# Performance work log

Measured on AMD Instinct MI355X. Metric: run time of the kernel, lower is better.

Reference implementation:

```python
import jax, jax.numpy as jnp
import numpy as np

EMBED_DIM = 1024
NUM_HEADS = 16
HEAD_DIM = EMBED_DIM // NUM_HEADS
NEG = -1000000000.0


def setup_inputs() -> dict:
    key = jax.random.key(0)
    ks = jax.random.split(key, 13)
    B, S, D = 4, 2048, EMBED_DIM
    scale = 1.0 / np.sqrt(D)
    inp = {
        "query": jax.random.normal(ks[0], (B, S, D), jnp.float32),
        "key": jax.random.normal(ks[1], (B, S, D), jnp.float32),
        "value": jax.random.normal(ks[2], (B, S, D), jnp.float32),
        "mask": jax.random.randint(ks[3], (B, 1, 1, S), 0, 2, jnp.int32),
        "Wq": jax.random.normal(ks[4], (D, D), jnp.float32) * scale,
        "bq": jnp.zeros((D,), jnp.float32),
        "Wk": jax.random.normal(ks[5], (D, D), jnp.float32) * scale,
        "bk": jnp.zeros((D,), jnp.float32),
        "Wv": jax.random.normal(ks[6], (D, D), jnp.float32) * scale,
        "bv": jnp.zeros((D,), jnp.float32),
        "Wo": jax.random.normal(ks[7], (D, D), jnp.float32) * scale,
        "bo": jnp.zeros((D,), jnp.float32),
    }
    return inp


def _split_heads(x):
    B, S, D = x.shape
    return x.reshape(B, S, NUM_HEADS, HEAD_DIM).transpose(0, 2, 1, 3)  # [B,H,S,hd]


def reference(query, key, value, mask, Wq, bq, Wk, bk, Wv, bv, Wo, bo):
    B, S, D = query.shape
    Q = _split_heads(query @ Wq + bq)
    K = _split_heads(key @ Wk + bk)
    V = _split_heads(value @ Wv + bv)
    scores = jnp.einsum("bhqd,bhkd->bhqk", Q, K) / jnp.sqrt(jnp.float32(HEAD_DIM))
    scores = jnp.where(mask == 0, jnp.float32(NEG), scores)
    attn = jax.nn.softmax(scores, axis=-1)
    out = jnp.einsum("bhqk,bhkd->bhqd", attn, V)
    out = out.transpose(0, 2, 1, 3).reshape(B, S, D)
    return out @ Wo + bo
```

## Files before the change

kernel.cpp:

```cpp
#include <hip/hip_runtime.h>


#define SEQ   2048
#define EDIM  1024
#define NHEAD 16
#define HDIM  64
#define NBAT  4
#define MTOK  8192

typedef __attribute__((ext_vector_type(8))) __bf16 bf16x8;
typedef __attribute__((ext_vector_type(4))) float f32x4;
typedef __attribute__((ext_vector_type(8))) unsigned short us8;
typedef unsigned short u16;

#define SCL   0.1803368801111244f
#define MADD_OK   (-12.0f)
#define MADD_MASK (-100000.0f)

__device__ __forceinline__ u16 bfbits(float f) {
    __bf16 h = (__bf16)f;
    return __builtin_bit_cast(u16, h);
}
__device__ __forceinline__ bf16x8 bc(us8 v) { return __builtin_bit_cast(bf16x8, v); }
__device__ __forceinline__ float exp2fast(float x) {
    float r;
    asm("v_exp_f32 %0, %1" : "=v"(r) : "v"(x));
    return r;
}

__global__ __launch_bounds__(256) void prep_kernel(const int* __restrict__ mask,
                                                   int* __restrict__ idxl,
                                                   int* __restrict__ cntp) {
    __shared__ int psum[257];
    const int b = blockIdx.x, t = threadIdx.x;
    const int* mp = mask + b * SEQ;
    int m8[8]; int s = 0;
#pragma unroll
    for (int i = 0; i < 8; ++i) { m8[i] = mp[t * 8 + i]; s += (m8[i] != 0); }
    psum[t + 1] = s;
    __syncthreads();
    if (t == 0) { psum[0] = 0; for (int i = 1; i <= 256; ++i) psum[i] += psum[i - 1]; }
    __syncthreads();
    int ex = psum[t];
#pragma unroll
    for (int i = 0; i < 8; ++i)
        if (m8[i] != 0) idxl[b * SEQ + (ex++)] = t * 8 + i;
    if (t == 0) cntp[b] = psum[256];
}

__global__ __launch_bounds__(256) void wtrans4_kernel(const float* __restrict__ W0,
                                                      const float* __restrict__ W1,
                                                      const float* __restrict__ W2,
                                                      const float* __restrict__ W3,
                                                      u16* __restrict__ WT) {
    __shared__ float tile[32][33];
    const int tx = threadIdx.x, ty = threadIdx.y;
    const int bx = blockIdx.x,  by = blockIdx.y, wz = blockIdx.z;
    const float* W = (wz == 0) ? W0 : (wz == 1) ? W1 : (wz == 2) ? W2 : W3;
    u16* O = WT + (size_t)wz * EDIM * EDIM;
#pragma unroll
    for (int i = 0; i < 4; ++i)
        tile[ty + i * 8][tx] = W[(size_t)(by * 32 + ty + i * 8) * EDIM + bx * 32 + tx];
    __syncthreads();
#pragma unroll
    for (int i = 0; i < 4; ++i) {
        int n = bx * 32 + ty + i * 8;
        int k = by * 32 + tx;
        O[(size_t)n * EDIM + k] = bfbits(tile[tx][ty + i * 8]);
    }
}

template <int MODE, bool ABF16, bool GATHER>
__global__ __launch_bounds__(256) void gemm_kernel(const void* __restrict__ Ap,
                                                   const u16* __restrict__ WT,
                                                   const float* __restrict__ bias,
                                                   void* __restrict__ outp,
                                                   const int* __restrict__ idxl,
                                                   const int* __restrict__ cntp) {
    const int bm = blockIdx.x, bn = blockIdx.y;
    int cn = 0;
    if constexpr (GATHER) {
        cn = cntp[bm >> 4];
        if (((bm & 15) * 128) >= cn) return;
    }

    __shared__ u16 As[128][56];
    __shared__ u16 Bs[128][56];

    const int tid  = threadIdx.x;
    const int lane = tid & 63, wave = tid >> 6;
    const int g    = lane >> 4, l15 = lane & 15;
    const int wrow = wave >> 1, wcol = wave & 1;
    const int tr   = tid >> 1, tk = (tid & 1) * 16;

    int arow;
    if constexpr (GATHER) {
        const int sloc = (bm & 15) * 128 + tr;
        const int gi = (sloc < cn) ? idxl[(bm >> 4) * SEQ + sloc] : 0;
        arow = (bm >> 4) * SEQ + gi;
    } else {
        arow = bm * 128 + tr;
    }

    f32x4 acc[4][4] = {};

    bf16x8 sa0, sa1, sb0, sb1;
    auto LOAD = [&](int k0) {
        if constexpr (ABF16) {
            const u16* A = (const u16*)Ap;
            const u16* p = A + (size_t)arow * EDIM + k0 + tk;
            sa0 = bc(*(const us8*)p);
            sa1 = bc(*(const us8*)(p + 8));
        } else {
            const float* A = (const float*)Ap;
            const float* p = A + (size_t)arow * EDIM + k0 + tk;
            f32x4 v0 = *(const f32x4*)p;
            f32x4 v1 = *(const f32x4*)(p + 4);
            f32x4 v2 = *(const f32x4*)(p + 8);
            f32x4 v3 = *(const f32x4*)(p + 12);
#pragma unroll
            for (int j = 0; j < 4; ++j) {
                sa0[j] = (__bf16)v0[j]; sa0[4 + j] = (__bf16)v1[j];
                sa1[j] = (__bf16)v2[j]; sa1[4 + j] = (__bf16)v3[j];
            }
        }
        const u16* q = WT + (size_t)(bn * 128 + tr) * EDIM + k0 + tk;
        sb0 = bc(*(const us8*)q);
        sb1 = bc(*(const us8*)(q + 8));
    };

    LOAD(0);
#pragma unroll 1
    for (int kt = 0; kt < EDIM / 32; ++kt) {
        __syncthreads();
        *(bf16x8*)&As[tr][tk]     = sa0;
        *(bf16x8*)&As[tr][tk + 8] = sa1;
        *(bf16x8*)&Bs[tr][tk]     = sb0;
        *(bf16x8*)&Bs[tr][tk + 8] = sb1;
        __syncthreads();
        if (kt < EDIM / 32 - 1) LOAD((kt + 1) * 32);

        bf16x8 af[4], bfr[4];
#pragma unroll
        for (int i = 0; i < 4; ++i)
            af[i] = bc(*(const us8*)&As[wrow * 64 + i * 16 + l15][g * 8]);
#pragma unroll
        for (int j = 0; j < 4; ++j)
            bfr[j] = bc(*(const us8*)&Bs[wcol * 64 + j * 16 + l15][g * 8]);
#pragma unroll
        for (int i = 0; i < 4; ++i)
#pragma unroll
            for (int j = 0; j < 4; ++j)
                acc[i][j] = __builtin_amdgcn_mfma_f32_16x16x32_bf16(af[i], bfr[j], acc[i][j], 0, 0, 0);
    }

#pragma unroll
    for (int i = 0; i < 4; ++i) {
#pragma unroll
        for (int j = 0; j < 4; ++j) {
            const int gm0 = bm * 128 + wrow * 64 + i * 16 + g * 4;
            const int gn  = bn * 128 + wcol * 64 + j * 16 + l15;
            const float bv = bias[gn];
#pragma unroll
            for (int r = 0; r < 4; ++r) {
                float val = acc[i][j][r] + bv;
                const int m = gm0 + r;
                if constexpr (GATHER) {
                    if ((m & 2047) >= cn) val = 0.f;
                }
                if constexpr (MODE == 2) {
                    ((float*)outp)[(size_t)m * EDIM + gn] = val;
                } else {
                    const int b = m >> 11, s = m & 2047;
                    const int h = gn >> 6, d = gn & 63;
                    u16* O = (u16*)outp;
                    if constexpr (MODE == 0)
                        O[((size_t)(b * NHEAD + h) << 17) + s * HDIM + d] = bfbits(val);
                    else
                        O[((size_t)(b * NHEAD + h) << 17) + d * SEQ + s] = bfbits(val);
                }
            }
        }
    }
}

__global__ __launch_bounds__(256) void attn_kernel(const u16* __restrict__ Q,
                                                   const u16* __restrict__ K,
                                                   const u16* __restrict__ VT,
                                                   const int* __restrict__ cntp,
                                                   u16* __restrict__ O) {
    __shared__ u16 Klds[2][64][72];
    __shared__ u16 Vlds[2][64][72];
    __shared__ float madd[SEQ];

    const int tid = threadIdx.x, lane = tid & 63, w = tid >> 6;
    const int g = lane >> 4, l15 = lane & 15;
    const int qb = blockIdx.x, bh = blockIdx.y;
    const int b = bh >> 4, h = bh & 15;

    const u16* Qp = Q + ((size_t)bh << 17);
    const u16* Kp = K + ((size_t)bh << 17);
    const u16* Vp = VT + ((size_t)bh << 17);
    const int q0 = qb * 64 + w * 16;

    const int cn  = cntp[b];
    const int ktc = (cn + 63) >> 6;

    for (int i = tid; i < ktc * 64; i += 256)
        madd[i] = (i < cn) ? MADD_OK : MADD_MASK;

    bf16x8 qf0 = bc(*(const us8*)&Qp[(size_t)(q0 + l15) * HDIM + g * 8]);
    bf16x8 qf1 = bc(*(const us8*)&Qp[(size_t)(q0 + l15) * HDIM + 32 + g * 8]);

    f32x4 ot[4] = {};
    float lsum = 0.f;

    const int sr = tid >> 2, scol = (tid & 3) * 16;
    const int kRow = ((l15 >> 2) << 3) + (l15 & 3);
    const f32x4 zf = {0.f, 0.f, 0.f, 0.f};

    {
        us8 a = *(const us8*)&Kp[(size_t)sr * HDIM + scol];
        us8 bq_ = *(const us8*)&Kp[(size_t)sr * HDIM + scol + 8];
        us8 c = *(const us8*)&Vp[(size_t)sr * SEQ + scol];
        us8 d = *(const us8*)&Vp[(size_t)sr * SEQ + scol + 8];
        *(us8*)&Klds[0][sr][scol]     = a;
        *(us8*)&Klds[0][sr][scol + 8] = bq_;
        *(us8*)&Vlds[0][sr][scol]     = c;
        *(us8*)&Vlds[0][sr][scol + 8] = d;
    }
    __syncthreads();

    for (int kt = 0; kt < ktc; ++kt) {
        const int cur = kt & 1;
        const int kbase = kt * 64;
        const bool more = (kt + 1) < ktc;

        us8 nk0, nk1, nv0, nv1;
        if (more) {
            const int nb = kbase + 64;
            nk0 = *(const us8*)&Kp[(size_t)(nb + sr) * HDIM + scol];
            nk1 = *(const us8*)&Kp[(size_t)(nb + sr) * HDIM + scol + 8];
            nv0 = *(const us8*)&Vp[(size_t)sr * SEQ + nb + scol];
            nv1 = *(const us8*)&Vp[(size_t)sr * SEQ + nb + scol + 8];
        }

        f32x4 st[4];
        const u16* Kb = &Klds[cur][0][0];
        __builtin_amdgcn_s_setprio(1);
#pragma unroll
        for (int u = 0; u < 4; ++u) {
            const int R = kRow + (u & 1) * 4 + (u >> 1) * 32;
            bf16x8 kf0 = bc(*(const us8*)&Kb[R * 72 + g * 8]);
            bf16x8 kf1 = bc(*(const us8*)&Kb[R * 72 + 32 + g * 8]);
            st[u] = __builtin_amdgcn_mfma_f32_16x16x32_bf16(kf0, qf0, zf, 0, 0, 0);
            st[u] = __builtin_amdgcn_mfma_f32_16x16x32_bf16(kf1, qf1, st[u], 0, 0, 0);
        }
        __builtin_amdgcn_s_setprio(0);

        float p[4][4];
#pragma unroll
        for (int u = 0; u < 4; ++u) {
            const f32x4 ma = *(const f32x4*)&madd[kbase + (u >> 1) * 32 + (u & 1) * 4 + g * 8];
#pragma unroll
            for (int r = 0; r < 4; ++r) {
                p[u][r] = exp2fast(fmaf(st[u][r], SCL, ma[r]));
                lsum += p[u][r];
            }
        }
        bf16x8 pf0, pf1;
#pragma unroll
        for (int j = 0; j < 4; ++j) {
            pf0[j]     = (__bf16)p[0][j];
            pf0[4 + j] = (__bf16)p[1][j];
            pf1[j]     = (__bf16)p[2][j];
            pf1[4 + j] = (__bf16)p[3][j];
        }

        const u16* Vb = &Vlds[cur][0][0];
        __builtin_amdgcn_s_setprio(1);
#pragma unroll
        for (int dblk = 0; dblk < 4; ++dblk) {
            bf16x8 vf0 = bc(*(const us8*)&Vb[(dblk * 16 + l15) * 72 + g * 8]);
            bf16x8 vf1 = bc(*(const us8*)&Vb[(dblk * 16 + l15) * 72 + 32 + g * 8]);
            ot[dblk] = __builtin_amdgcn_mfma_f32_16x16x32_bf16(vf0, pf0, ot[dblk], 0, 0, 0);
            ot[dblk] = __builtin_amdgcn_mfma_f32_16x16x32_bf16(vf1, pf1, ot[dblk], 0, 0, 0);
        }
        __builtin_amdgcn_s_setprio(0);

        if (more) {
            *(us8*)&Klds[cur ^ 1][sr][scol]     = nk0;
            *(us8*)&Klds[cur ^ 1][sr][scol + 8] = nk1;
            *(us8*)&Vlds[cur ^ 1][sr][scol]     = nv0;
            *(us8*)&Vlds[cur ^ 1][sr][scol + 8] = nv1;
        }
        __syncthreads();
    }

    lsum += __shfl_xor(lsum, 16);
    lsum += __shfl_xor(lsum, 32);
    const float inv = 1.f / lsum;

    const size_t row = (size_t)(b * SEQ + q0 + l15) * EDIM + h * HDIM;
#pragma unroll
    for (int dblk = 0; dblk < 4; ++dblk) {
#pragma unroll
        for (int j = 0; j < 2; ++j) {
            __attribute__((ext_vector_type(2))) __bf16 pr;
            pr[0] = (__bf16)(ot[dblk][2 * j] * inv);
            pr[1] = (__bf16)(ot[dblk][2 * j + 1] * inv);
            *(unsigned*)&O[row + dblk * 16 + g * 4 + 2 * j] = __builtin_bit_cast(unsigned, pr);
        }
    }
}

extern "C" void kernel_launch(void* const* d_in, const int* in_sizes, int n_in,
                              void* d_out, int out_size, void* d_ws, size_t ws_size,
                              hipStream_t stream) {
    const float* query = (const float*)d_in[0];
    const float* key   = (const float*)d_in[1];
    const float* value = (const float*)d_in[2];
    const int*   mask  = (const int*)d_in[3];
    const float* Wq = (const float*)d_in[4];  const float* bq = (const float*)d_in[5];
    const float* Wk = (const float*)d_in[6];  const float* bk = (const float*)d_in[7];
    const float* Wv = (const float*)d_in[8];  const float* bv = (const float*)d_in[9];
    const float* Wo = (const float*)d_in[10]; const float* bo = (const float*)d_in[11];

    char* ws = (char*)d_ws;
    const size_t WT_BYTES  = (size_t)EDIM * EDIM * 2;
    const size_t BUF_BYTES = (size_t)MTOK * EDIM * 2;
    u16* wtq   = (u16*)(ws);
    u16* wtk   = (u16*)(ws + WT_BYTES);
    u16* wtv   = (u16*)(ws + 2 * WT_BYTES);
    u16* wto   = (u16*)(ws + 3 * WT_BYTES);
    u16* Qbuf  = (u16*)(ws + 4 * WT_BYTES);
    u16* Kbuf  = (u16*)(ws + 4 * WT_BYTES + BUF_BYTES);
    u16* VTbuf = (u16*)(ws + 4 * WT_BYTES + 2 * BUF_BYTES);
    u16* Abuf  = (u16*)(ws + 4 * WT_BYTES + 3 * BUF_BYTES);
    int* idxl  = (int*)(ws + 4 * WT_BYTES + 4 * BUF_BYTES);
    int* cntp  = (int*)(ws + 4 * WT_BYTES + 4 * BUF_BYTES + (size_t)MTOK * 4);

    prep_kernel<<<NBAT, 256, 0, stream>>>(mask, idxl, cntp);

    dim3 tgrid(32, 32, 4), tblk(32, 8);
    wtrans4_kernel<<<tgrid, tblk, 0, stream>>>(Wq, Wk, Wv, Wo, wtq);

    dim3 ggrid(MTOK / 128, EDIM / 128);
    gemm_kernel<0, false, false><<<ggrid, 256, 0, stream>>>(query, wtq, bq, Qbuf, nullptr, nullptr);
    gemm_kernel<0, false, true ><<<ggrid, 256, 0, stream>>>(key,   wtk, bk, Kbuf, idxl, cntp);
    gemm_kernel<1, false, true ><<<ggrid, 256, 0, stream>>>(value, wtv, bv, VTbuf, idxl, cntp);

    dim3 agrid(SEQ / 64, NBAT * NHEAD);
    attn_kernel<<<agrid, 256, 0, stream>>>(Qbuf, Kbuf, VTbuf, cntp, Abuf);

    gemm_kernel<2, true, false><<<ggrid, 256, 0, stream>>>(Abuf, wto, bo, (float*)d_out, nullptr, nullptr);
}
```

Baseline: 215.7 us.

## Use 32x32x16 MFMA with XOR-swizzled LDS and remapped block order in attention

Rewrites the attention kernel to use 32x32x16 bf16 MFMA instructions, with each wave owning 32 query rows instead of 16. The block therefore covers 128 queries. The padded LDS tiles are replaced by unpadded 64x64 tiles with XOR swizzles to avoid bank conflicts. Blocks are launched as a 1D grid with a remap so that neighbouring blocks in launch order come from different batch-head pairs. The aim is to halve the K/V LDS traffic per query and reduce MFMA instruction count, at the cost of more accumulator registers and half as many blocks.

```diff
diff --git a/kernel.cpp b/kernel.cpp
--- a/kernel.cpp
+++ b/kernel.cpp
@@ -9,7 +9,9 @@
 #define MTOK  8192
 
 typedef __attribute__((ext_vector_type(8))) __bf16 bf16x8;
+typedef __attribute__((ext_vector_type(4))) __bf16 bf16x4;
 typedef __attribute__((ext_vector_type(4))) float f32x4;
+typedef __attribute__((ext_vector_type(16))) float f32x16;
 typedef __attribute__((ext_vector_type(8))) unsigned short us8;
 typedef unsigned short u16;
 
@@ -189,19 +191,22 @@
                                                    const u16* __restrict__ VT,
                                                    const int* __restrict__ cntp,
                                                    u16* __restrict__ O) {
-    __shared__ u16 Klds[2][64][72];
-    __shared__ u16 Vlds[2][64][72];
+    __shared__ u16 Klds[2][64][64];
+    __shared__ u16 Vlds[2][64][64];
     __shared__ float madd[SEQ];
 
     const int tid = threadIdx.x, lane = tid & 63, w = tid >> 6;
-    const int g = lane >> 4, l15 = lane & 15;
-    const int qb = blockIdx.x, bh = blockIdx.y;
-    const int b = bh >> 4, h = bh & 15;
+    const int h = lane >> 5, l31 = lane & 31;
+
+    const int id  = blockIdx.x;
+    const int bh  = (id & 7) * 8 + ((id >> 3) >> 4);
+    const int qb  = (id >> 3) & 15;
+    const int b   = bh >> 4, hd_ = bh & 15;
 
     const u16* Qp = Q + ((size_t)bh << 17);
     const u16* Kp = K + ((size_t)bh << 17);
     const u16* Vp = VT + ((size_t)bh << 17);
-    const int q0 = qb * 64 + w * 16;
+    const int q0w = qb * 128 + w * 32;
 
     const int cn  = cntp[b];
     const int ktc = (cn + 63) >> 6;
@@ -209,25 +214,34 @@
     for (int i = tid; i < ktc * 64; i += 256)
         madd[i] = (i < cn) ? MADD_OK : MADD_MASK;
 
-    bf16x8 qf0 = bc(*(const us8*)&Qp[(size_t)(q0 + l15) * HDIM + g * 8]);
-    bf16x8 qf1 = bc(*(const us8*)&Qp[(size_t)(q0 + l15) * HDIM + 32 + g * 8]);
-
-    f32x4 ot[4] = {};
+    bf16x8 qf[4];
+#pragma unroll
+    for (int khd = 0; khd < 4; ++khd)
+        qf[khd] = bc(*(const us8*)&Qp[(size_t)(q0w + l31) * HDIM + khd * 16 + h * 8]);
+
+    const int b_  = l31 & 3, hp = (l31 >> 2) & 1, cc = l31 >> 3;
+    const int piR = 16 * (cc & 1) + 8 * hp + 4 * (cc >> 1) + b_;
+    const int swk = (piR & 3) ^ (((piR >> 3) & 3) << 1);
+    const int swv = l31 & 7;
+
+    const int sr = tid >> 2, cu = (tid & 3) * 16;
+    const int ksw = ((sr & 3) ^ (((sr >> 3) & 3) << 1)) << 3;
+    const int vsw = (sr & 7) << 3;
+    const int kc0 = cu ^ ksw, kc1 = (cu + 8) ^ ksw;
+    const int vc0 = cu ^ vsw, vc1 = (cu + 8) ^ vsw;
+
+    f32x16 ot[2] = {};
     float lsum = 0.f;
 
-    const int sr = tid >> 2, scol = (tid & 3) * 16;
-    const int kRow = ((l15 >> 2) << 3) + (l15 & 3);
-    const f32x4 zf = {0.f, 0.f, 0.f, 0.f};
-
     {
-        us8 a = *(const us8*)&Kp[(size_t)sr * HDIM + scol];
-        us8 bq_ = *(const us8*)&Kp[(size_t)sr * HDIM + scol + 8];
-        us8 c = *(const us8*)&Vp[(size_t)sr * SEQ + scol];
-        us8 d = *(const us8*)&Vp[(size_t)sr * SEQ + scol + 8];
-        *(us8*)&Klds[0][sr][scol]     = a;
-        *(us8*)&Klds[0][sr][scol + 8] = bq_;
-        *(us8*)&Vlds[0][sr][scol]     = c;
-        *(us8*)&Vlds[0][sr][scol + 8] = d;
+        us8 a0 = *(const us8*)&Kp[(size_t)sr * HDIM + cu];
+        us8 a1 = *(const us8*)&Kp[(size_t)sr * HDIM + cu + 8];
+        us8 a2 = *(const us8*)&Vp[(size_t)sr * SEQ + cu];
+        us8 a3 = *(const us8*)&Vp[(size_t)sr * SEQ + cu + 8];
+        *(us8*)&Klds[0][sr][kc0] = a0;
+        *(us8*)&Klds[0][sr][kc1] = a1;
+        *(us8*)&Vlds[0][sr][vc0] = a2;
+        *(us8*)&Vlds[0][sr][vc1] = a3;
     }
     __syncthreads();
 
@@ -239,77 +253,85 @@
         us8 nk0, nk1, nv0, nv1;
         if (more) {
             const int nb = kbase + 64;
-            nk0 = *(const us8*)&Kp[(size_t)(nb + sr) * HDIM + scol];
-            nk1 = *(const us8*)&Kp[(size_t)(nb + sr) * HDIM + scol + 8];
-            nv0 = *(const us8*)&Vp[(size_t)sr * SEQ + nb + scol];
-            nv1 = *(const us8*)&Vp[(size_t)sr * SEQ + nb + scol + 8];
-        }
-
-        f32x4 st[4];
-        const u16* Kb = &Klds[cur][0][0];
+            nk0 = *(const us8*)&Kp[(size_t)(nb + sr) * HDIM + cu];
+            nk1 = *(const us8*)&Kp[(size_t)(nb + sr) * HDIM + cu + 8];
+            nv0 = *(const us8*)&Vp[(size_t)sr * SEQ + nb + cu];
+            nv1 = *(const us8*)&Vp[(size_t)sr * SEQ + nb + cu + 8];
+        }
+
+        f32x16 st[2] = {};
         __builtin_amdgcn_s_setprio(1);
 #pragma unroll
-        for (int u = 0; u < 4; ++u) {
-            const int R = kRow + (u & 1) * 4 + (u >> 1) * 32;
-            bf16x8 kf0 = bc(*(const us8*)&Kb[R * 72 + g * 8]);
-            bf16x8 kf1 = bc(*(const us8*)&Kb[R * 72 + 32 + g * 8]);
-            st[u] = __builtin_amdgcn_mfma_f32_16x16x32_bf16(kf0, qf0, zf, 0, 0, 0);
-            st[u] = __builtin_amdgcn_mfma_f32_16x16x32_bf16(kf1, qf1, st[u], 0, 0, 0);
+        for (int kb2 = 0; kb2 < 2; ++kb2) {
+            const u16* Kr = &Klds[cur][kb2 * 32 + piR][0];
+#pragma unroll
+            for (int khd = 0; khd < 4; ++khd) {
+                bf16x8 kf = bc(*(const us8*)&Kr[(khd * 16 + h * 8) ^ (swk << 3)]);
+                st[kb2] = __builtin_amdgcn_mfma_f32_32x32x16_bf16(kf, qf[khd], st[kb2], 0, 0, 0);
+            }
         }
         __builtin_amdgcn_s_setprio(0);
 
-        float p[4][4];
-#pragma unroll
-        for (int u = 0; u < 4; ++u) {
-            const f32x4 ma = *(const f32x4*)&madd[kbase + (u >> 1) * 32 + (u & 1) * 4 + g * 8];
-#pragma unroll
-            for (int r = 0; r < 4; ++r) {
-                p[u][r] = exp2fast(fmaf(st[u][r], SCL, ma[r]));
-                lsum += p[u][r];
-            }
-        }
-        bf16x8 pf0, pf1;
-#pragma unroll
-        for (int j = 0; j < 4; ++j) {
-            pf0[j]     = (__bf16)p[0][j];
-            pf0[4 + j] = (__bf16)p[1][j];
-            pf1[j]     = (__bf16)p[2][j];
-            pf1[4 + j] = (__bf16)p[3][j];
-        }
-
-        const u16* Vb = &Vlds[cur][0][0];
+        float pv[2][16];
+#pragma unroll
+        for (int kb2 = 0; kb2 < 2; ++kb2) {
+#pragma unroll
+            for (int cp = 0; cp < 4; ++cp) {
+                const f32x4 ma = *(const f32x4*)&madd[kbase + kb2 * 32 + 16 * (cp & 1) + 4 * (cp >> 1) + 8 * h];
+#pragma unroll
+                for (int j = 0; j < 4; ++j) {
+                    const float pe = exp2fast(fmaf(st[kb2][cp * 4 + j], SCL, ma[j]));
+                    pv[kb2][cp * 4 + j] = pe;
+                    lsum += pe;
+                }
+            }
+        }
+
+        bf16x8 pf[4];
+#pragma unroll
+        for (int s = 0; s < 4; ++s) {
+            const int kb2 = s >> 1, sel = (s & 1) * 4;
+#pragma unroll
+            for (int j = 0; j < 4; ++j) {
+                pf[s][j]     = (__bf16)pv[kb2][sel + j];
+                pf[s][4 + j] = (__bf16)pv[kb2][8 + sel + j];
+            }
+        }
+
         __builtin_amdgcn_s_setprio(1);
 #pragma unroll
-        for (int dblk = 0; dblk < 4; ++dblk) {
-            bf16x8 vf0 = bc(*(const us8*)&Vb[(dblk * 16 + l15) * 72 + g * 8]);
-            bf16x8 vf1 = bc(*(const us8*)&Vb[(dblk * 16 + l15) * 72 + 32 + g * 8]);
-            ot[dblk] = __builtin_amdgcn_mfma_f32_16x16x32_bf16(vf0, pf0, ot[dblk], 0, 0, 0);
-            ot[dblk] = __builtin_amdgcn_mfma_f32_16x16x32_bf16(vf1, pf1, ot[dblk], 0, 0, 0);
+        for (int dblk = 0; dblk < 2; ++dblk) {
+            const u16* Vr = &Vlds[cur][dblk * 32 + l31][0];
+#pragma unroll
+            for (int s = 0; s < 4; ++s) {
+                bf16x8 vf = bc(*(const us8*)&Vr[(s * 16 + h * 8) ^ (swv << 3)]);
+                ot[dblk] = __builtin_amdgcn_mfma_f32_32x32x16_bf16(vf, pf[s], ot[dblk], 0, 0, 0);
+            }
         }
         __builtin_amdgcn_s_setprio(0);
 
         if (more) {
-            *(us8*)&Klds[cur ^ 1][sr][scol]     = nk0;
-            *(us8*)&Klds[cur ^ 1][sr][scol + 8] = nk1;
-            *(us8*)&Vlds[cur ^ 1][sr][scol]     = nv0;
-            *(us8*)&Vlds[cur ^ 1][sr][scol + 8] = nv1;
+            *(us8*)&Klds[cur ^ 1][sr][kc0] = nk0;
+            *(us8*)&Klds[cur ^ 1][sr][kc1] = nk1;
+            *(us8*)&Vlds[cur ^ 1][sr][vc0] = nv0;
+            *(us8*)&Vlds[cur ^ 1][sr][vc1] = nv1;
         }
         __syncthreads();
     }
 
-    lsum += __shfl_xor(lsum, 16);
     lsum += __shfl_xor(lsum, 32);
     const float inv = 1.f / lsum;
 
-    const size_t row = (size_t)(b * SEQ + q0 + l15) * EDIM + h * HDIM;
-#pragma unroll
-    for (int dblk = 0; dblk < 4; ++dblk) {
-#pragma unroll
-        for (int j = 0; j < 2; ++j) {
-            __attribute__((ext_vector_type(2))) __bf16 pr;
-            pr[0] = (__bf16)(ot[dblk][2 * j] * inv);
-            pr[1] = (__bf16)(ot[dblk][2 * j + 1] * inv);
-            *(unsigned*)&O[row + dblk * 16 + g * 4 + 2 * j] = __builtin_bit_cast(unsigned, pr);
+    const size_t row = (size_t)(b * SEQ + q0w + l31) * EDIM + hd_ * HDIM;
+#pragma unroll
+    for (int dblk = 0; dblk < 2; ++dblk) {
+#pragma unroll
+        for (int cp = 0; cp < 4; ++cp) {
+            bf16x4 t;
+#pragma unroll
+            for (int j = 0; j < 4; ++j)
+                t[j] = (__bf16)(ot[dblk][cp * 4 + j] * inv);
+            *(bf16x4*)&O[row + dblk * 32 + 8 * cp + 4 * h] = t;
         }
     }
 }
@@ -350,8 +372,7 @@
     gemm_kernel<0, false, true ><<<ggrid, 256, 0, stream>>>(key,   wtk, bk, Kbuf, idxl, cntp);
     gemm_kernel<1, false, true ><<<ggrid, 256, 0, stream>>>(value, wtv, bv, VTbuf, idxl, cntp);
 
-    dim3 agrid(SEQ / 64, NBAT * NHEAD);
-    attn_kernel<<<agrid, 256, 0, stream>>>(Qbuf, Kbuf, VTbuf, cntp, Abuf);
+    attn_kernel<<<1024, 256, 0, stream>>>(Qbuf, Kbuf, VTbuf, cntp, Abuf);
 
     gemm_kernel<2, true, false><<<ggrid, 256, 0, stream>>>(Abuf, wto, bo, (float*)d_out, nullptr, nullptr);
 }
```

New measurement: 205.8 us. 4.6% less time.
